# Kernel optimization log

Hardware: AMD Instinct MI355X
Metric: run time of the kernel (lower is better)

## Reference

```python
import jax, jax.numpy as jnp
import numpy as np

N_NODES = 100000
N_EDGES = 1600000
N_DATE = 5000  # last N_DATE nodes are date nodes [0,0,1]
D_IN = 128
D_H = 128
N_CLASSES = 16
MLP_HID = 8


def setup_inputs() -> dict:
    key = jax.random.key(0)
    ks = jax.random.split(key, 12)
    feature = jax.random.normal(ks[0], (N_NODES, D_IN), dtype=jnp.float32)
    edge_weight = jax.random.uniform(ks[1], (N_EDGES,), dtype=jnp.float32)
    src = jax.random.randint(ks[2], (N_EDGES,), 0, N_NODES, dtype=jnp.int32)
    dst = jax.random.randint(ks[3], (N_EDGES,), 0, N_NODES, dtype=jnp.int32)
    # node_type one-hot: regular nodes [1,0,0], last N_DATE nodes are date nodes [0,0,1]
    nt = np.zeros((N_NODES, 3), dtype=np.int32)
    nt[: N_NODES - N_DATE, 0] = 1
    nt[N_NODES - N_DATE :, 2] = 1
    node_type = jnp.asarray(nt)
    # GraphConv weights (xavier uniform) + zero bias, DGL convention: h @ W, W:[in,out]
    def xavier(k, fan_in, fan_out):
        lim = float(np.sqrt(6.0 / (fan_in + fan_out)))
        return jax.random.uniform(k, (fan_in, fan_out), jnp.float32, -lim, lim)
    W0 = xavier(ks[4], D_IN, D_H)
    b0 = jnp.zeros((D_H,), jnp.float32)
    W1 = xavier(ks[5], D_H, D_H)
    b1 = jnp.zeros((D_H,), jnp.float32)
    mlp_w1 = xavier(ks[6], D_H, MLP_HID)
    mlp_b1 = jnp.zeros((MLP_HID,), jnp.float32)
    mlp_w2 = xavier(ks[7], MLP_HID, N_CLASSES)
    mlp_b2 = jnp.zeros((N_CLASSES,), jnp.float32)
    return {
        "feature": feature, "edge_weight": edge_weight, "src": src, "dst": dst,
        "node_type": node_type, "W0": W0, "b0": b0, "W1": W1, "b1": b1,
        "mlp_w1": mlp_w1, "mlp_b1": mlp_b1, "mlp_w2": mlp_w2, "mlp_b2": mlp_b2,
    }


def reference(feature, edge_weight, src, dst, node_type,
              W0, b0, W1, b1, mlp_w1, mlp_b1, mlp_w2, mlp_b2):
    n = feature.shape[0]
    ones_e = jnp.ones_like(edge_weight)
    # unweighted degrees (DGL norm='both'), clamped to >= 1
    deg_out = jnp.clip(jax.ops.segment_sum(ones_e, src, num_segments=n), 1.0)
    deg_in = jnp.clip(jax.ops.segment_sum(ones_e, dst, num_segments=n), 1.0)
    norm_src = deg_out ** -0.5  # [N]
    norm_dst = deg_in ** -0.5   # [N]

    def graph_conv(h, W, b):
        hn = h * norm_src[:, None]                      # D_out^{-1/2} src scaling
        msg = hn[src] * edge_weight[:, None]            # [E, d] edge-weighted gather
        agg = jax.ops.segment_sum(msg, dst, num_segments=n)  # scatter-add
        return (agg * norm_dst[:, None]) @ W + b        # D_in^{-1/2}, then linear

    h = jax.nn.relu(graph_conv(feature, W0, b0))
    h = jax.nn.relu(graph_conv(h, W1, b1))

    # sum-pool over date nodes ([0,0,1]) == tail slice in original layout
    date_mask = ((node_type[:, 0] == 0) & (node_type[:, 1] == 0) & (node_type[:, 2] == 1)).astype(h.dtype)
    cnt = date_mask.sum()
    pooled = (h * date_mask[:, None]).sum(axis=0) / cnt  # [d_h]

    hid = jax.nn.relu(pooled @ mlp_w1 + mlp_b1)
    return hid @ mlp_w2 + mlp_b2  # [num_classes]
```

## Files before the change

kernel.cpp:

```cpp
#include <hip/hip_runtime.h>
#include <hip/hip_fp16.h>
#include <hip/hip_fp8.h>
#include <stdint.h>

#define D 128
#define GT 16
#define SLOTS 48
#define EPB 4096
#define PTB 1024
#define CAPE 5120
#define MAXB 400
#define MAXDATE 8192
#define WPN 16384
#define PWAVES 8

typedef _Float16 f16x8 __attribute__((ext_vector_type(8)));
typedef float    f32x4 __attribute__((ext_vector_type(4)));
typedef float    f32x2 __attribute__((ext_vector_type(2)));

__global__ __launch_bounds__(PTB) void partition_kernel(
    const int* __restrict__ src, const int* __restrict__ dst, const float* __restrict__ ew,
    int* __restrict__ cursorA, int* __restrict__ cursorB,
    int2* __restrict__ ebuf, int* __restrict__ sbuf, int E, int nbk) {
    __shared__ int histA[MAXB], histB[MAXB], baseA[MAXB], baseB[MAXB];
    int tid = threadIdx.x;
    for (int i = tid; i < nbk; i += PTB) { histA[i] = 0; histB[i] = 0; }
    __syncthreads();
    int e0 = blockIdx.x * EPB;
    int dcache[EPB / PTB], scache[EPB / PTB];
    float wcache[EPB / PTB];
    #pragma unroll
    for (int i = 0; i < EPB / PTB; ++i) {
        int e = e0 + i * PTB + tid;
        bool ok = e < E;
        dcache[i] = ok ? dst[e] : -1;
        scache[i] = ok ? src[e] : 0;
        wcache[i] = ok ? ew[e] : 0.f;
        if (ok) {
            atomicAdd(&histA[dcache[i] >> 8], 1);
            atomicAdd(&histB[scache[i] >> 8], 1);
        }
    }
    __syncthreads();
    for (int i = tid; i < nbk; i += PTB) {
        baseA[i] = atomicAdd(&cursorA[i], histA[i]);
        baseB[i] = atomicAdd(&cursorB[i], histB[i]);
        histA[i] = 0; histB[i] = 0;
    }
    __syncthreads();
    #pragma unroll
    for (int i = 0; i < EPB / PTB; ++i) {
        if (dcache[i] >= 0) {
            int d = dcache[i], s = scache[i];
            int bA = d >> 8;
            int pA = baseA[bA] + atomicAdd(&histA[bA], 1);
            if (pA < CAPE) ebuf[(size_t)bA * CAPE + pA] =
                make_int2(s | ((d & 255) << 17), __float_as_int(wcache[i]));
            int bB = s >> 8;
            int pB = baseB[bB] + atomicAdd(&histB[bB], 1);
            if (pB < CAPE) sbuf[(size_t)bB * CAPE + pB] = s;
        }
    }
}

__global__ __launch_bounds__(256) void build_count_kernel(
    const int2* __restrict__ ebuf, const int* __restrict__ cursorA,
    const int* __restrict__ sbuf, const int* __restrict__ cursorB,
    int2* __restrict__ ell, int* __restrict__ deg_in, int* __restrict__ deg_out,
    int n, int nbk) {
    __shared__ int lcur[256];
    int tid = threadIdx.x;
    lcur[tid] = 0;
    __syncthreads();
    if (blockIdx.x < (unsigned)nbk) {
        int b = blockIdx.x;
        int cntE = min(cursorA[b], CAPE);
        const int2* buf = ebuf + (size_t)b * CAPE;
        for (int i = tid; i < cntE; i += 256) {
            int2 r = buf[i];
            int s = r.x & 0x1FFFF;
            int dlow = (r.x >> 17) & 255;
            int slot = atomicAdd(&lcur[dlow], 1);
            int node = (b << 8) + dlow;
            if (slot < SLOTS) ell[(size_t)node * SLOTS + slot] = make_int2(s, r.y);
        }
        __syncthreads();
        int v = (b << 8) + tid;
        if (v < n) deg_in[v] = lcur[tid];
    } else {
        int b = blockIdx.x - nbk;
        int cntS = min(cursorB[b], CAPE);
        const int* buf = sbuf + (size_t)b * CAPE;
        for (int i = tid; i < cntS; i += 256) {
            atomicAdd(&lcur[buf[i] & 255], 1);
        }
        __syncthreads();
        int v = (b << 8) + tid;
        if (v < n) deg_out[v] = lcur[tid];
    }
}

__global__ void norm_flag_kernel(const int* __restrict__ deg_out, const int* __restrict__ deg_in,
                                 const int* __restrict__ node_type,
                                 float* __restrict__ norm_src, float* __restrict__ norm_dst,
                                 int* __restrict__ list, int* __restrict__ cnt,
                                 unsigned char* __restrict__ flag, int n) {
    int v = blockIdx.x * blockDim.x + threadIdx.x;
    if (v < n) {
        float d_o = (float)max(deg_out[v], 1);
        float d_i = (float)max(deg_in[v], 1);
        norm_src[v] = 1.0f / sqrtf(d_o);
        norm_dst[v] = 1.0f / sqrtf(d_i);
        flag[v] = 0;
        int t0 = node_type[v * 3 + 0];
        int t1 = node_type[v * 3 + 1];
        int t2 = node_type[v * 3 + 2];
        if (t0 == 0 && t1 == 0 && t2 == 1) {
            int idx = atomicAdd(cnt, 1);
            list[idx] = v;
        }
    }
}

__global__ __launch_bounds__(256) void mark_kernel(
    const int* __restrict__ list, const int* __restrict__ cnt,
    const int2* __restrict__ ell, const int* __restrict__ deg_in,
    unsigned char* __restrict__ flag) {
    int wave = (blockIdx.x * 256 + threadIdx.x) >> 6;
    int lane = threadIdx.x & 63;
    if (wave >= min(*cnt, MAXDATE)) return;
    int v = __builtin_amdgcn_readfirstlane(list[wave]);
    int m = min(deg_in[v], SLOTS);
    if (lane < m) {
        int s = ell[(size_t)v * SLOTS + lane].x;
        flag[s] = 1;
    }
}

__global__ __launch_bounds__(256) void compact_kernel(
    const unsigned char* __restrict__ flag, const int* __restrict__ deg_in,
    int* __restrict__ list2, int* __restrict__ cnt2, int n) {
    int v = blockIdx.x * 256 + threadIdx.x;
    int lane = threadIdx.x & 63;
    bool f = (v < n) && (flag[v] != 0);
    unsigned long long mask = __ballot(f);
    int base = 0;
    if (lane == 0 && mask) base = atomicAdd(cnt2, __popcll(mask));
    base = __shfl(base, 0);
    if (f) {
        int off = __builtin_amdgcn_mbcnt_hi((unsigned int)(mask >> 32),
                  __builtin_amdgcn_mbcnt_lo((unsigned int)mask, 0));
        list2[base + off] = v | (min(deg_in[v], SLOTS) << 17);
    }
}

__global__ __launch_bounds__(256) void wpack_kernel(const float* __restrict__ W,
                                                    _Float16* __restrict__ wp,
                                                    int* __restrict__ cursorAB,
                                                    float* __restrict__ pooled,
                                                    int* __restrict__ cnt) {
    int tid = threadIdx.x;
    if (blockIdx.x == 0) {
        for (int i = tid; i < 2 * MAXB; i += 256) cursorAB[i] = 0;
        if (tid < D) pooled[tid] = 0.f;
        if (tid == 0) { cnt[0] = 0; cnt[1] = 0; }
    }
    int base = blockIdx.x * 256 + tid;
    for (int idx = base; idx < WPN; idx += gridDim.x * 256) {
        int j = idx & 7;
        int l = (idx >> 3) & 63;
        int c = (idx >> 9) & 7;
        int k0b = idx >> 12;
        int q = l >> 4, r = l & 15;
        float w = W[(k0b * 32 + q * 8 + j) * 128 + c * 16 + r];
        _Float16 hi = (_Float16)w;
        wp[idx] = hi;
        wp[idx + WPN] = (_Float16)(w - (float)hi);
    }
}

__global__ __launch_bounds__(256) void gemm_mfma_kernel(
    const float* __restrict__ X, const float* __restrict__ ns,
    const _Float16* __restrict__ wp, unsigned char* __restrict__ P8, int n) {
    int lane = threadIdx.x & 63;
    int wib  = threadIdx.x >> 6;
    int q = lane >> 4, r = lane & 15;
    int row0 = blockIdx.x * 64 + wib * 16;
    if (row0 >= n) return;
    int ra = min(row0 + r, n - 1);
    float sa = ns[ra];

    float4 x[8];
    #pragma unroll
    for (int kb = 0; kb < 4; ++kb) {
        x[2 * kb]     = *(const float4*)&X[(size_t)ra * 128 + kb * 32 + q * 8];
        x[2 * kb + 1] = *(const float4*)&X[(size_t)ra * 128 + kb * 32 + q * 8 + 4];
    }
    f16x8 a[4];
    #pragma unroll
    for (int kb = 0; kb < 4; ++kb) {
        a[kb][0] = (_Float16)(x[2 * kb].x * sa);
        a[kb][1] = (_Float16)(x[2 * kb].y * sa);
        a[kb][2] = (_Float16)(x[2 * kb].z * sa);
        a[kb][3] = (_Float16)(x[2 * kb].w * sa);
        a[kb][4] = (_Float16)(x[2 * kb + 1].x * sa);
        a[kb][5] = (_Float16)(x[2 * kb + 1].y * sa);
        a[kb][6] = (_Float16)(x[2 * kb + 1].z * sa);
        a[kb][7] = (_Float16)(x[2 * kb + 1].w * sa);
    }

    f32x4 acc[8];
    #pragma unroll
    for (int c = 0; c < 8; ++c) acc[c] = (f32x4){0.f, 0.f, 0.f, 0.f};

    const _Float16* wb = wp + lane * 8;
    #pragma unroll
    for (int c = 0; c < 8; ++c) {
        #pragma unroll
        for (int kb = 0; kb < 4; ++kb) {
            f16x8 bh = *(const f16x8*)&wb[kb * 4096 + c * 512];
            f16x8 bl = *(const f16x8*)&wb[kb * 4096 + c * 512 + WPN];
            acc[c] = __builtin_amdgcn_mfma_f32_16x16x32_f16(bh, a[kb], acc[c], 0, 0, 0);
            acc[c] = __builtin_amdgcn_mfma_f32_16x16x32_f16(bl, a[kb], acc[c], 0, 0, 0);
        }
    }

    int row = row0 + r;
    if (row < n) {
        #pragma unroll
        for (int c = 0; c < 8; ++c) {
            int w0 = __builtin_amdgcn_cvt_pk_fp8_f32(acc[c][0], acc[c][1], 0, false);
            int w1 = __builtin_amdgcn_cvt_pk_fp8_f32(acc[c][2], acc[c][3], w0, true);
            *(unsigned int*)&P8[(size_t)row * 128 + c * 16 + q * 4] = (unsigned int)w1;
        }
    }
}

__global__ __launch_bounds__(256) void gather1_kernel(
    const unsigned char* __restrict__ P8, const int2* __restrict__ ell,
    const float* __restrict__ norm_src, const float* __restrict__ norm_dst,
    const float* __restrict__ bias, const int* __restrict__ list2,
    const int* __restrict__ cnt2, __half* __restrict__ h1) {
    int wave = (blockIdx.x * 256 + threadIdx.x) >> 6;
    int lane = threadIdx.x & 63;
    int nn = __builtin_amdgcn_readfirstlane(*cnt2);
    if (wave >= nn) return;
    int pk = __builtin_amdgcn_readfirstlane(list2[wave]);
    int v = pk & 0x1FFFF;
    int m = pk >> 17;
    int half = lane >> 5;
    int l32  = lane & 31;
    const int2* row = ell + (size_t)v * SLOTS;
    const unsigned int* P32 = (const unsigned int*)P8;
    float nd = norm_dst[v];
    float ns = norm_src[v];
    float4 acc = make_float4(0.f, 0.f, 0.f, 0.f);

    if (m <= 16) {
        int4 q[8];
        #pragma unroll
        for (int i = 0; i < 8; ++i) q[i] = *(const int4*)&row[2 * i];
        unsigned int r[8];
        float w[8];
        #pragma unroll
        for (int i = 0; i < 8; ++i) {
            bool ok = (2 * i + half) < m;
            int s = ok ? (half ? q[i].z : q[i].x) : 0;
            w[i] = ok ? __int_as_float(half ? q[i].w : q[i].y) : 0.f;
            r[i] = P32[(size_t)s * 32 + l32];
        }
        #pragma unroll
        for (int i = 0; i < 8; ++i) {
            f32x2 c0 = __builtin_amdgcn_cvt_pk_f32_fp8((int)r[i], false);
            f32x2 c1 = __builtin_amdgcn_cvt_pk_f32_fp8((int)r[i], true);
            acc.x = fmaf(w[i], c0[0], acc.x);
            acc.y = fmaf(w[i], c0[1], acc.y);
            acc.z = fmaf(w[i], c1[0], acc.z);
            acc.w = fmaf(w[i], c1[1], acc.w);
        }
    } else {
        int4 q[16];
        #pragma unroll
        for (int i = 0; i < 16; ++i) q[i] = *(const int4*)&row[2 * i];
        unsigned int r[16];
        float w[16];
        #pragma unroll
        for (int i = 0; i < 16; ++i) {
            bool ok = (2 * i + half) < m;
            int s = ok ? (half ? q[i].z : q[i].x) : 0;
            w[i] = ok ? __int_as_float(half ? q[i].w : q[i].y) : 0.f;
            r[i] = P32[(size_t)s * 32 + l32];
        }
        #pragma unroll
        for (int i = 0; i < 16; ++i) {
            f32x2 c0 = __builtin_amdgcn_cvt_pk_f32_fp8((int)r[i], false);
            f32x2 c1 = __builtin_amdgcn_cvt_pk_f32_fp8((int)r[i], true);
            acc.x = fmaf(w[i], c0[0], acc.x);
            acc.y = fmaf(w[i], c0[1], acc.y);
            acc.z = fmaf(w[i], c1[0], acc.z);
            acc.w = fmaf(w[i], c1[1], acc.w);
        }
        if (m > 32) {
            for (int e = 32; e < m; e += 4) {
                int4 qa = *(const int4*)&row[e];
                int4 qb = *(const int4*)&row[e + 2];
                int2 p0 = half ? make_int2(qa.z, qa.w) : make_int2(qa.x, qa.y);
                int2 p1 = half ? make_int2(qb.z, qb.w) : make_int2(qb.x, qb.y);
                bool v0 = (e + half) < m;
                bool v1 = (e + 2 + half) < m;
                int s0 = v0 ? p0.x : 0;
                int s1 = v1 ? p1.x : 0;
                unsigned int r0 = P32[(size_t)s0 * 32 + l32];
                unsigned int r1 = P32[(size_t)s1 * 32 + l32];
                float w0 = v0 ? __int_as_float(p0.y) : 0.f;
                float w1 = v1 ? __int_as_float(p1.y) : 0.f;
                f32x2 c0 = __builtin_amdgcn_cvt_pk_f32_fp8((int)r0, false);
                f32x2 c1 = __builtin_amdgcn_cvt_pk_f32_fp8((int)r0, true);
                f32x2 d0 = __builtin_amdgcn_cvt_pk_f32_fp8((int)r1, false);
                f32x2 d1 = __builtin_amdgcn_cvt_pk_f32_fp8((int)r1, true);
                acc.x = fmaf(w0, c0[0], acc.x); acc.x = fmaf(w1, d0[0], acc.x);
                acc.y = fmaf(w0, c0[1], acc.y); acc.y = fmaf(w1, d0[1], acc.y);
                acc.z = fmaf(w0, c1[0], acc.z); acc.z = fmaf(w1, d1[0], acc.z);
                acc.w = fmaf(w0, c1[1], acc.w); acc.w = fmaf(w1, d1[1], acc.w);
            }
        }
    }

    acc.x += __shfl_xor(acc.x, 32);
    acc.y += __shfl_xor(acc.y, 32);
    acc.z += __shfl_xor(acc.z, 32);
    acc.w += __shfl_xor(acc.w, 32);
    if (half == 0) {
        float4 b4 = ((const float4*)bias)[l32];
        float ra = fmaxf(fmaf(acc.x, nd, b4.x), 0.f) * ns;
        float rb = fmaxf(fmaf(acc.y, nd, b4.y), 0.f) * ns;
        float rc = fmaxf(fmaf(acc.z, nd, b4.z), 0.f) * ns;
        float rd = fmaxf(fmaf(acc.w, nd, b4.w), 0.f) * ns;
        __half2 h0 = __floats2half2_rn(ra, rb);
        __half2 h1v = __floats2half2_rn(rc, rd);
        uint2 u;
        u.x = *(unsigned int*)&h0;
        u.y = *(unsigned int*)&h1v;
        ((uint2*)h1)[(size_t)v * 32 + l32] = u;
    }
}

__global__ __launch_bounds__(256) void gather2_list_kernel(
    const __half* __restrict__ h, const int* __restrict__ deg_in,
    const int2* __restrict__ ell, const float* __restrict__ norm_dst,
    const int* __restrict__ list, const int* __restrict__ cnt,
    float* __restrict__ out) {
    int wave = (blockIdx.x * 256 + threadIdx.x) >> 6;
    int lane = threadIdx.x & 63;
    if (wave >= min(*cnt, MAXDATE)) return;
    int v = __builtin_amdgcn_readfirstlane(list[wave]);
    int half = lane >> 5;
    int l32  = lane & 31;
    const int2* row = ell + (size_t)v * SLOTS;
    int dg = deg_in[v];
    int4 q[16];
    #pragma unroll
    for (int i = 0; i < 16; ++i) q[i] = *(const int4*)&row[2 * i];
    int m = min(dg, SLOTS);
    float2 r[16];
    float w[16];
    #pragma unroll
    for (int i = 0; i < 16; ++i) {
        bool ok = (2 * i + half) < m;
        int s = ok ? (half ? q[i].z : q[i].x) : 0;
        w[i] = ok ? __int_as_float(half ? q[i].w : q[i].y) : 0.f;
        r[i] = ((const float2*)h)[(size_t)s * 32 + l32];
    }
    float4 acc = make_float4(0.f, 0.f, 0.f, 0.f);
    #pragma unroll
    for (int i = 0; i < 16; ++i) {
        float2 a01 = __half22float2(*(const __half2*)&r[i].x);
        float2 a23 = __half22float2(*(const __half2*)&r[i].y);
        acc.x = fmaf(w[i], a01.x, acc.x);
        acc.y = fmaf(w[i], a01.y, acc.y);
        acc.z = fmaf(w[i], a23.x, acc.z);
        acc.w = fmaf(w[i], a23.y, acc.w);
    }
    if (m > 32) {
        for (int e = 32; e < m; e += 4) {
            int4 qa = *(const int4*)&row[e];
            int4 qb = *(const int4*)&row[e + 2];
            int2 p0 = half ? make_int2(qa.z, qa.w) : make_int2(qa.x, qa.y);
            int2 p1 = half ? make_int2(qb.z, qb.w) : make_int2(qb.x, qb.y);
            bool v0 = (e + half) < m;
            bool v1 = (e + 2 + half) < m;
            int s0 = v0 ? p0.x : 0;
            int s1 = v1 ? p1.x : 0;
            float2 raw0 = ((const float2*)h)[(size_t)s0 * 32 + l32];
            float2 raw1 = ((const float2*)h)[(size_t)s1 * 32 + l32];
            float w0 = v0 ? __int_as_float(p0.y) : 0.f;
            float w1 = v1 ? __int_as_float(p1.y) : 0.f;
            float2 a01 = __half22float2(*(const __half2*)&raw0.x);
            float2 a23 = __half22float2(*(const __half2*)&raw0.y);
            float2 b01 = __half22float2(*(const __half2*)&raw1.x);
            float2 b23 = __half22float2(*(const __half2*)&raw1.y);
            acc.x = fmaf(w0, a01.x, acc.x); acc.x = fmaf(w1, b01.x, acc.x);
            acc.y = fmaf(w0, a01.y, acc.y); acc.y = fmaf(w1, b01.y, acc.y);
            acc.z = fmaf(w0, a23.x, acc.z); acc.z = fmaf(w1, b23.x, acc.z);
            acc.w = fmaf(w0, a23.y, acc.w); acc.w = fmaf(w1, b23.y, acc.w);
        }
    }
    acc.x += __shfl_xor(acc.x, 32);
    acc.y += __shfl_xor(acc.y, 32);
    acc.z += __shfl_xor(acc.z, 32);
    acc.w += __shfl_xor(acc.w, 32);
    if (half == 0) {
        float nd = norm_dst[v];
        ((float4*)(out + (size_t)wave * D))[l32] =
            make_float4(acc.x * nd, acc.y * nd, acc.z * nd, acc.w * nd);
    }
}

__global__ __launch_bounds__(512) void gemm_pool_kernel(
    const float* __restrict__ X, const float* __restrict__ W,
    const float* __restrict__ bias, const int* __restrict__ cnt,
    float* __restrict__ pooled) {
    __shared__ float wlds[D * D];
    __shared__ float rows[PWAVES][GT * D];
    int tid  = threadIdx.x;
    int lane = tid & 63;
    int wib  = tid >> 6;

    const float4* W4 = (const float4*)W;
    for (int i = tid; i < (D * D) / 4; i += 512)
        *(float4*)&wlds[i * 4] = W4[i];
    __syncthreads();

    int m = min(*cnt, MAXDATE);
    int ntiles = (m + GT - 1) / GT;
    float2 bb = ((const float2*)bias)[lane];
    float psx = 0.f, psy = 0.f;
    bool any = false;
    float* rw = rows[wib];
    const float2* X2 = (const float2*)X;

    for (int tile = blockIdx.x * PWAVES + wib; tile < ntiles; tile += gridDim.x * PWAVES) {
        int t0 = tile * GT;
        any = true;
        #pragma unroll
        for (int t = 0; t < GT; ++t) {
            int i = t0 + t;
            float2 r = (i < m) ? X2[(size_t)i * 64 + lane] : make_float2(0.f, 0.f);
            *(float2*)&rw[t * D + 2 * lane] = r;
        }
        __builtin_amdgcn_wave_barrier();

        float2 acc[GT];
        #pragma unroll
        for (int t = 0; t < GT; ++t) acc[t] = make_float2(0.f, 0.f);

        for (int k = 0; k < D; k += 4) {
            float2 w0 = *(const float2*)&wlds[(k + 0) * D + 2 * lane];
            float2 w1 = *(const float2*)&wlds[(k + 1) * D + 2 * lane];
            float2 w2 = *(const float2*)&wlds[(k + 2) * D + 2 * lane];
            float2 w3 = *(const float2*)&wlds[(k + 3) * D + 2 * lane];
            #pragma unroll
            for (int t = 0; t < GT; ++t) {
                float4 r = *(const float4*)&rw[t * D + k];
                acc[t].x = fmaf(r.x, w0.x, acc[t].x); acc[t].y = fmaf(r.x, w0.y, acc[t].y);
                acc[t].x = fmaf(r.y, w1.x, acc[t].x); acc[t].y = fmaf(r.y, w1.y, acc[t].y);
                acc[t].x = fmaf(r.z, w2.x, acc[t].x); acc[t].y = fmaf(r.z, w2.y, acc[t].y);
                acc[t].x = fmaf(r.w, w3.x, acc[t].x); acc[t].y = fmaf(r.w, w3.y, acc[t].y);
            }
        }

        #pragma unroll
        for (int t = 0; t < GT; ++t) {
            if (t0 + t < m) {
                psx += fmaxf(acc[t].x + bb.x, 0.f);
                psy += fmaxf(acc[t].y + bb.y, 0.f);
            }
        }
        __builtin_amdgcn_wave_barrier();
    }

    if (any) {
        atomicAdd(&pooled[2 * lane + 0], psx);
        atomicAdd(&pooled[2 * lane + 1], psy);
    }
}

__global__ void mlp_kernel(const float* __restrict__ pooled, const int* __restrict__ cnt,
                           const float* __restrict__ w1, const float* __restrict__ b1,
                           const float* __restrict__ w2, const float* __restrict__ b2,
                           float* __restrict__ out) {
    __shared__ float hid[8];
    int t = threadIdx.x;
    float inv = 1.0f / (float)(*cnt);
    if (t < 8) {
        float a = b1[t];
        for (int k = 0; k < 128; ++k) a = fmaf(pooled[k] * inv, w1[k * 8 + t], a);
        hid[t] = fmaxf(a, 0.f);
    }
    __syncthreads();
    if (t < 16) {
        float a = b2[t];
        for (int j = 0; j < 8; ++j) a = fmaf(hid[j], w2[j * 16 + t], a);
        out[t] = a;
    }
}

extern "C" void kernel_launch(void* const* d_in, const int* in_sizes, int n_in,
                              void* d_out, int out_size, void* d_ws, size_t ws_size,
                              hipStream_t stream) {
    const float* feature   = (const float*)d_in[0];
    const float* ew        = (const float*)d_in[1];
    const int*   src       = (const int*)d_in[2];
    const int*   dst       = (const int*)d_in[3];
    const int*   node_type = (const int*)d_in[4];
    const float* W0        = (const float*)d_in[5];
    const float* b0        = (const float*)d_in[6];
    const float* W1        = (const float*)d_in[7];
    const float* b1        = (const float*)d_in[8];
    const float* mw1       = (const float*)d_in[9];
    const float* mb1       = (const float*)d_in[10];
    const float* mw2       = (const float*)d_in[11];
    const float* mb2       = (const float*)d_in[12];
    float* out = (float*)d_out;

    const int n = in_sizes[0] / D;
    const int E = in_sizes[1];
    const int NBK = (n + 255) >> 8;

    char* ws = (char*)d_ws;
    size_t off = 0;
    auto alloc = [&](size_t bytes) -> void* {
        void* p = ws + off;
        off = (off + bytes + 255) & ~(size_t)255;
        return p;
    };
    int*           cursorAB = (int*)alloc(2 * MAXB * 4);
    int*           deg_in   = (int*)alloc((size_t)n * 4);
    int*           deg_out  = (int*)alloc((size_t)n * 4);
    float*         norm_src = (float*)alloc((size_t)n * 4);
    float*         norm_dst = (float*)alloc((size_t)n * 4);
    int*           list     = (int*)alloc((size_t)n * 4);
    int*           list2    = (int*)alloc((size_t)n * 4);
    unsigned char* flag     = (unsigned char*)alloc((size_t)n);
    int2*          ell      = (int2*)alloc(((size_t)n * SLOTS + 8) * 8);
    int2*          ebuf     = (int2*)alloc((size_t)NBK * CAPE * 8);
    int*           sbuf     = (int*)alloc((size_t)NBK * CAPE * 4);
    unsigned char* P8       = (unsigned char*)alloc((size_t)n * D);
    __half*        h1       = (__half*)alloc((size_t)n * D * 2);
    _Float16*      wp       = (_Float16*)alloc(2 * WPN * 2);
    float*         pooled   = (float*)alloc(D * 4);
    int*           cnt      = (int*)alloc(256);
    float*         agg      = (float*)sbuf;

    int* cursorA = cursorAB;
    int* cursorB = cursorAB + MAXB;
    int* cnt2    = cnt + 1;

    const int TB = 256;
    int pblk = (E + EPB - 1) / EPB;
    int nblk = (n + TB - 1) / TB;

    wpack_kernel<<<16, TB, 0, stream>>>(W0, wp, cursorAB, pooled, cnt);
    partition_kernel<<<pblk, PTB, 0, stream>>>(src, dst, ew, cursorA, cursorB, ebuf, sbuf, E, NBK);
    build_count_kernel<<<2 * NBK, TB, 0, stream>>>(ebuf, cursorA, sbuf, cursorB,
                                                   ell, deg_in, deg_out, n, NBK);
    norm_flag_kernel<<<nblk, TB, 0, stream>>>(deg_out, deg_in, node_type,
                                              norm_src, norm_dst, list, cnt, flag, n);
    mark_kernel<<<(MAXDATE * 64) / TB, TB, 0, stream>>>(list, cnt, ell, deg_in, flag);
    compact_kernel<<<nblk, TB, 0, stream>>>(flag, deg_in, list2, cnt2, n);

    gemm_mfma_kernel<<<(n + 63) / 64, TB, 0, stream>>>(feature, norm_src, wp, P8, n);

    gather1_kernel<<<(n * 64 + TB - 1) / TB, TB, 0, stream>>>(
        P8, ell, norm_src, norm_dst, b0, list2, cnt2, h1);

    gather2_list_kernel<<<(MAXDATE * 64) / TB, TB, 0, stream>>>(
        h1, deg_in, ell, norm_dst, list, cnt, agg);
    gemm_pool_kernel<<<64, 512, 0, stream>>>(agg, W1, b1, cnt, pooled);

    mlp_kernel<<<1, 64, 0, stream>>>(pooled, cnt, mw1, mb1, mw2, mb2, out);
}
```

Baseline: 284.2 us.

## Replace two-pass bucket partition with direct global-atomic ELL scatter

Replaces the partition and build_count kernels, which bucketed edges in shared memory and then built the ELL table per bucket, with one kernel. That kernel does global atomicAdd on deg_in and deg_out per edge and writes each edge straight into its ELL slot. It removes one launch and the intermediate ebuf/sbuf round trip. In exchange it adds 3.2M global atomics with random addresses, and the zeroing of the degree arrays moves into wpack. Slot order within a node now depends on atomic timing, so float summation order may not be deterministic.

```diff
diff --git a/kernel.cpp b/kernel.cpp
--- a/kernel.cpp
+++ b/kernel.cpp
@@ -6,10 +6,6 @@
 #define D 128
 #define GT 16
 #define SLOTS 48
-#define EPB 4096
-#define PTB 1024
-#define CAPE 5120
-#define MAXB 400
 #define MAXDATE 8192
 #define WPN 16384
 #define PWAVES 8
@@ -18,85 +14,33 @@
 typedef float    f32x4 __attribute__((ext_vector_type(4)));
 typedef float    f32x2 __attribute__((ext_vector_type(2)));
 
-__global__ __launch_bounds__(PTB) void partition_kernel(
+__global__ __launch_bounds__(256) void scatter_ell_kernel(
     const int* __restrict__ src, const int* __restrict__ dst, const float* __restrict__ ew,
-    int* __restrict__ cursorA, int* __restrict__ cursorB,
-    int2* __restrict__ ebuf, int* __restrict__ sbuf, int E, int nbk) {
-    __shared__ int histA[MAXB], histB[MAXB], baseA[MAXB], baseB[MAXB];
-    int tid = threadIdx.x;
-    for (int i = tid; i < nbk; i += PTB) { histA[i] = 0; histB[i] = 0; }
-    __syncthreads();
-    int e0 = blockIdx.x * EPB;
-    int dcache[EPB / PTB], scache[EPB / PTB];
-    float wcache[EPB / PTB];
-    #pragma unroll
-    for (int i = 0; i < EPB / PTB; ++i) {
-        int e = e0 + i * PTB + tid;
-        bool ok = e < E;
-        dcache[i] = ok ? dst[e] : -1;
-        scache[i] = ok ? src[e] : 0;
-        wcache[i] = ok ? ew[e] : 0.f;
-        if (ok) {
-            atomicAdd(&histA[dcache[i] >> 8], 1);
-            atomicAdd(&histB[scache[i] >> 8], 1);
-        }
-    }
-    __syncthreads();
-    for (int i = tid; i < nbk; i += PTB) {
-        baseA[i] = atomicAdd(&cursorA[i], histA[i]);
-        baseB[i] = atomicAdd(&cursorB[i], histB[i]);
-        histA[i] = 0; histB[i] = 0;
-    }
-    __syncthreads();
-    #pragma unroll
-    for (int i = 0; i < EPB / PTB; ++i) {
-        if (dcache[i] >= 0) {
-            int d = dcache[i], s = scache[i];
-            int bA = d >> 8;
-            int pA = baseA[bA] + atomicAdd(&histA[bA], 1);
-            if (pA < CAPE) ebuf[(size_t)bA * CAPE + pA] =
-                make_int2(s | ((d & 255) << 17), __float_as_int(wcache[i]));
-            int bB = s >> 8;
-            int pB = baseB[bB] + atomicAdd(&histB[bB], 1);
-            if (pB < CAPE) sbuf[(size_t)bB * CAPE + pB] = s;
-        }
-    }
-}
-
-__global__ __launch_bounds__(256) void build_count_kernel(
-    const int2* __restrict__ ebuf, const int* __restrict__ cursorA,
-    const int* __restrict__ sbuf, const int* __restrict__ cursorB,
-    int2* __restrict__ ell, int* __restrict__ deg_in, int* __restrict__ deg_out,
-    int n, int nbk) {
-    __shared__ int lcur[256];
-    int tid = threadIdx.x;
-    lcur[tid] = 0;
-    __syncthreads();
-    if (blockIdx.x < (unsigned)nbk) {
-        int b = blockIdx.x;
-        int cntE = min(cursorA[b], CAPE);
-        const int2* buf = ebuf + (size_t)b * CAPE;
-        for (int i = tid; i < cntE; i += 256) {
-            int2 r = buf[i];
-            int s = r.x & 0x1FFFF;
-            int dlow = (r.x >> 17) & 255;
-            int slot = atomicAdd(&lcur[dlow], 1);
-            int node = (b << 8) + dlow;
-            if (slot < SLOTS) ell[(size_t)node * SLOTS + slot] = make_int2(s, r.y);
-        }
-        __syncthreads();
-        int v = (b << 8) + tid;
-        if (v < n) deg_in[v] = lcur[tid];
+    int2* __restrict__ ell, int* __restrict__ deg_in, int* __restrict__ deg_out, int E) {
+    int t = blockIdx.x * 256 + threadIdx.x;
+    int base = t * 4;
+    if (base + 3 < E) {
+        int4 s4 = *(const int4*)&src[base];
+        int4 d4 = *(const int4*)&dst[base];
+        float4 w4 = *(const float4*)&ew[base];
+        int ss[4] = {s4.x, s4.y, s4.z, s4.w};
+        int dd[4] = {d4.x, d4.y, d4.z, d4.w};
+        float ww[4] = {w4.x, w4.y, w4.z, w4.w};
+        #pragma unroll
+        for (int i = 0; i < 4; ++i) {
+            int slot = atomicAdd(&deg_in[dd[i]], 1);
+            if (slot < SLOTS)
+                ell[(size_t)dd[i] * SLOTS + slot] = make_int2(ss[i], __float_as_int(ww[i]));
+            atomicAdd(&deg_out[ss[i]], 1);
+        }
     } else {
-        int b = blockIdx.x - nbk;
-        int cntS = min(cursorB[b], CAPE);
-        const int* buf = sbuf + (size_t)b * CAPE;
-        for (int i = tid; i < cntS; i += 256) {
-            atomicAdd(&lcur[buf[i] & 255], 1);
-        }
-        __syncthreads();
-        int v = (b << 8) + tid;
-        if (v < n) deg_out[v] = lcur[tid];
+        for (int e = base; e < E; ++e) {
+            int s = src[e], d = dst[e];
+            float w = ew[e];
+            int slot = atomicAdd(&deg_in[d], 1);
+            if (slot < SLOTS) ell[(size_t)d * SLOTS + slot] = make_int2(s, __float_as_int(w));
+            atomicAdd(&deg_out[s], 1);
+        }
     }
 }
 
@@ -156,17 +100,19 @@
 
 __global__ __launch_bounds__(256) void wpack_kernel(const float* __restrict__ W,
                                                     _Float16* __restrict__ wp,
-                                                    int* __restrict__ cursorAB,
+                                                    int* __restrict__ deg_in,
+                                                    int* __restrict__ deg_out,
                                                     float* __restrict__ pooled,
-                                                    int* __restrict__ cnt) {
+                                                    int* __restrict__ cnt, int n) {
     int tid = threadIdx.x;
+    int gt  = blockIdx.x * 256 + tid;
+    int gsz = gridDim.x * 256;
     if (blockIdx.x == 0) {
-        for (int i = tid; i < 2 * MAXB; i += 256) cursorAB[i] = 0;
         if (tid < D) pooled[tid] = 0.f;
         if (tid == 0) { cnt[0] = 0; cnt[1] = 0; }
     }
-    int base = blockIdx.x * 256 + tid;
-    for (int idx = base; idx < WPN; idx += gridDim.x * 256) {
+    for (int i = gt; i < n; i += gsz) { deg_in[i] = 0; deg_out[i] = 0; }
+    for (int idx = gt; idx < WPN; idx += gsz) {
         int j = idx & 7;
         int l = (idx >> 3) & 63;
         int c = (idx >> 9) & 7;
@@ -525,7 +471,6 @@
 
     const int n = in_sizes[0] / D;
     const int E = in_sizes[1];
-    const int NBK = (n + 255) >> 8;
 
     char* ws = (char*)d_ws;
     size_t off = 0;
@@ -534,7 +479,6 @@
         off = (off + bytes + 255) & ~(size_t)255;
         return p;
     };
-    int*           cursorAB = (int*)alloc(2 * MAXB * 4);
     int*           deg_in   = (int*)alloc((size_t)n * 4);
     int*           deg_out  = (int*)alloc((size_t)n * 4);
     float*         norm_src = (float*)alloc((size_t)n * 4);
@@ -543,27 +487,21 @@
     int*           list2    = (int*)alloc((size_t)n * 4);
     unsigned char* flag     = (unsigned char*)alloc((size_t)n);
     int2*          ell      = (int2*)alloc(((size_t)n * SLOTS + 8) * 8);
-    int2*          ebuf     = (int2*)alloc((size_t)NBK * CAPE * 8);
-    int*           sbuf     = (int*)alloc((size_t)NBK * CAPE * 4);
     unsigned char* P8       = (unsigned char*)alloc((size_t)n * D);
     __half*        h1       = (__half*)alloc((size_t)n * D * 2);
     _Float16*      wp       = (_Float16*)alloc(2 * WPN * 2);
     float*         pooled   = (float*)alloc(D * 4);
     int*           cnt      = (int*)alloc(256);
-    float*         agg      = (float*)sbuf;
-
-    int* cursorA = cursorAB;
-    int* cursorB = cursorAB + MAXB;
-    int* cnt2    = cnt + 1;
+    float*         agg      = (float*)alloc((size_t)MAXDATE * D * 4);
+
+    int* cnt2 = cnt + 1;
 
     const int TB = 256;
-    int pblk = (E + EPB - 1) / EPB;
     int nblk = (n + TB - 1) / TB;
-
-    wpack_kernel<<<16, TB, 0, stream>>>(W0, wp, cursorAB, pooled, cnt);
-    partition_kernel<<<pblk, PTB, 0, stream>>>(src, dst, ew, cursorA, cursorB, ebuf, sbuf, E, NBK);
-    build_count_kernel<<<2 * NBK, TB, 0, stream>>>(ebuf, cursorA, sbuf, cursorB,
-                                                   ell, deg_in, deg_out, n, NBK);
+    int eblk = (E / 4 + TB - 1) / TB;
+
+    wpack_kernel<<<16, TB, 0, stream>>>(W0, wp, deg_in, deg_out, pooled, cnt, n);
+    scatter_ell_kernel<<<eblk, TB, 0, stream>>>(src, dst, ew, ell, deg_in, deg_out, E);
     norm_flag_kernel<<<nblk, TB, 0, stream>>>(deg_out, deg_in, node_type,
                                               norm_src, norm_dst, list, cnt, flag, n);
     mark_kernel<<<(MAXDATE * 64) / TB, TB, 0, stream>>>(list, cnt, ell, deg_in, flag);
```

Result: slower. 387.7 us (+36.4%).
